# Kernel optimization log

Measured on AMD Instinct MI355X. Metric: run time of the kernel, lower is better.

The kernel has to match this reference:

```python
import jax, jax.numpy as jnp
import numpy as np

K = 7  # number of relaxed nearest neighbors (init arg k)
EXPM1_GUARD = 1e-7
LOG_HALF = float(np.log(0.5))

def log1mexp(x):
    # log(1 - exp(x)) for x <= 0, numerically stable (guard matches torch bw-path constant)
    t = x < LOG_HALF
    xa = jnp.where(t, x, -1.0)          # safe operand for log1p(-exp(.))
    xb = jnp.where(t, -1.0, x)          # safe operand for log(-expm1(.))
    ya = jnp.log1p(-jnp.exp(xa))
    yb = jnp.log(-jnp.expm1(xb) + EXPM1_GUARD)
    return jnp.where(t, ya, yb)

def setup_inputs() -> dict:
    key = jax.random.key(0)
    k1, k2, k3, k4 = jax.random.split(key, 4)
    b, n, m, o, e, f = 4, 8192, 2048, 64, 64, 128
    x = jax.random.normal(k1, (b, n, f), dtype=jnp.float32)
    xe = jax.random.normal(k2, (b, n, e), dtype=jnp.float32)
    ye = jax.random.normal(k3, (b, m, e), dtype=jnp.float32)
    log_temp_param = jnp.zeros((1,), dtype=jnp.float32)
    I = jax.random.randint(k4, (b, m, o), 0, n, dtype=jnp.int64)
    return {"x": x, "xe": xe, "ye": ye, "log_temp_param": log_temp_param, "I": I}

def reference(x, xe, ye, log_temp_param, I):
    b, n, f = x.shape
    m, o = I.shape[1], I.shape[2]
    bidx = jnp.arange(b)[:, None, None]          # [b,1,1] batch index for gathers

    # ---- compute_distances (indexed path): D[b,m,o] = -||xe[I] - ye||^2 ----
    xg_e = xe[bidx, I]                           # [b,m,o,e] gathered candidate embeddings
    diff = xg_e - ye[:, :, None, :]              # [b,m,o,e]
    D = -jnp.sum(diff * diff, axis=-1)           # [b,m,o]

    # ---- NeuralNearestNeighbors: temperature + k-step relaxed top-k ----
    temperature = jnp.exp(log_temp_param[0])     # log_temp_bias = log(1) = 0
    logits = (D / temperature).reshape(b * m, o)
    samples = []
    for _ in range(K):
        w = jax.nn.log_softmax(logits, axis=1)   # [b*m,o]
        samples.append(jnp.exp(w).reshape(b, m, o))
        logits = logits + log1mexp(w)
    W = jnp.stack(samples, axis=3)               # [b,m,o,K]

    # ---- aggregate_output: z[b,m,f,K] = sum_o W[b,m,o,K] * x[b, I[b,m,o], f] ----
    xg = x[bidx, I]                              # [b,m,o,f]
    z = jnp.einsum('bmok,bmof->bmfk', W, xg)     # [b,m,f,K]
    return z
```

## Files before the change

### kernel.cpp

```cpp
#include <hip/hip_runtime.h>
#include <math.h>

#define B_  4
#define N_  8192
#define M_  2048
#define O_  64
#define E_  64
#define F_  128
#define K_  7

__global__ __launch_bounds__(128, 6) void n3agg_kernel(
    const float* __restrict__ x, const float* __restrict__ xe,
    const float* __restrict__ ye, const float* __restrict__ log_temp,
    const int* __restrict__ I, float* __restrict__ out)
{
    __shared__ __align__(16) int   s_I[2][O_];
    __shared__ __align__(16) float s_ye[2][E_];
    __shared__ __align__(16) float s_W[2][O_][8];

    const int tid  = threadIdx.x;
    const int w    = tid >> 6;
    const int lane = tid & 63;
    const int bid  = blockIdx.x * 2 + w;
    const int b    = bid >> 11;

    const int my_idx = I[(size_t)bid * O_ + lane];
    s_I[w][lane]  = my_idx;
    s_ye[w][lane] = ye[(size_t)bid * E_ + lane];

    const float4* xr4 = (const float4*)(xe + ((size_t)b * N_ + my_idx) * E_);
    const float4* ye4 = (const float4*)(&s_ye[w][0]);
    float S[16];
    #pragma unroll
    for (int q = 0; q < 4; ++q) {
        float4 xa = xr4[q],      ya = ye4[q];
        float4 xb = xr4[q + 4],  yb = ye4[q + 4];
        float4 xc = xr4[q + 8],  yc = ye4[q + 8];
        float4 xd = xr4[q + 12], yd = ye4[q + 12];
        float da, db, dc, dd;

        da = __fsub_rn(xa.x, ya.x); db = __fsub_rn(xb.x, yb.x);
        dc = __fsub_rn(xc.x, yc.x); dd = __fsub_rn(xd.x, yd.x);
        S[4*q+0] = __fadd_rn(__fadd_rn(__fmul_rn(da,da), __fmul_rn(db,db)),
                             __fadd_rn(__fmul_rn(dc,dc), __fmul_rn(dd,dd)));

        da = __fsub_rn(xa.y, ya.y); db = __fsub_rn(xb.y, yb.y);
        dc = __fsub_rn(xc.y, yc.y); dd = __fsub_rn(xd.y, yd.y);
        S[4*q+1] = __fadd_rn(__fadd_rn(__fmul_rn(da,da), __fmul_rn(db,db)),
                             __fadd_rn(__fmul_rn(dc,dc), __fmul_rn(dd,dd)));

        da = __fsub_rn(xa.z, ya.z); db = __fsub_rn(xb.z, yb.z);
        dc = __fsub_rn(xc.z, yc.z); dd = __fsub_rn(xd.z, yd.z);
        S[4*q+2] = __fadd_rn(__fadd_rn(__fmul_rn(da,da), __fmul_rn(db,db)),
                             __fadd_rn(__fmul_rn(dc,dc), __fmul_rn(dd,dd)));

        da = __fsub_rn(xa.w, ya.w); db = __fsub_rn(xb.w, yb.w);
        dc = __fsub_rn(xc.w, yc.w); dd = __fsub_rn(xd.w, yd.w);
        S[4*q+3] = __fadd_rn(__fadd_rn(__fmul_rn(da,da), __fmul_rn(db,db)),
                             __fadd_rn(__fmul_rn(dc,dc), __fmul_rn(dd,dd)));
    }
    float t8[8], t4[4], t2[2], res;
    #pragma unroll
    for (int l = 0; l < 8; ++l) t8[l] = __fadd_rn(S[l], S[l + 8]);
    #pragma unroll
    for (int l = 0; l < 4; ++l) t4[l] = __fadd_rn(t8[l], t8[l + 4]);
    t2[0] = __fadd_rn(t4[0], t4[2]);
    t2[1] = __fadd_rn(t4[1], t4[3]);
    res   = __fadd_rn(t2[0], t2[1]);

    const float temp = expf(log_temp[0]);
    float logit = __fdiv_rn(-res, temp);

    float wreg[K_];
    #pragma unroll
    for (int k = 0; k < K_; ++k) {
        float mx = logit;
        #pragma unroll
        for (int d = 1; d < 64; d <<= 1) mx = fmaxf(mx, __shfl_xor(mx, d));
        float sh = __fsub_rn(logit, mx);
        float ex = expf(sh);
        float t = __fadd_rn(ex, __shfl_xor(ex, 16));
        t = __fadd_rn(t, __shfl_xor(t, 32));
        t = __fadd_rn(t, __shfl_xor(t, 8));
        t = __fadd_rn(t, __shfl_xor(t, 4));
        t = __fadd_rn(t, __shfl_xor(t, 2));
        t = __fadd_rn(t, __shfl_xor(t, 1));
        const float sm = t;

        float wv = __fsub_rn(sh, logf(sm));
        wreg[k] = expf(wv);

        float lm;
        if (wv < -0.69314718055994530942f) {
            lm = log1pf(-expf(wv));
        } else {
            lm = logf(__fadd_rn(-expm1f(wv), 1e-7f));
        }
        logit = __fadd_rn(logit, lm);
    }
    {
        float* wp = &s_W[w][lane][0];
        *(float4*)wp       = make_float4(wreg[0], wreg[1], wreg[2], wreg[3]);
        *(float2*)(wp + 4) = make_float2(wreg[4], wreg[5]);
        wp[6] = wreg[6];
    }

    const int h  = lane >> 5;
    const int fl = lane & 31;
    float acc[4][K_];
    #pragma unroll
    for (int q = 0; q < 4; ++q)
        #pragma unroll
        for (int k = 0; k < K_; ++k) acc[q][k] = 0.f;

    const float* xb = x + (size_t)b * N_ * F_ + 4 * fl;
    #pragma unroll 2
    for (int t = 0; t < 32; ++t) {
        const int o = 2 * t + h;
        const int idx = s_I[w][o];
        const float4 xv = *(const float4*)(xb + (size_t)idx * F_);
        const float* wrow = &s_W[w][o][0];
        const float4 wa = *(const float4*)(wrow);
        const float4 wb = *(const float4*)(wrow + 4);
        const float wk[K_] = {wa.x, wa.y, wa.z, wa.w, wb.x, wb.y, wb.z};
        #pragma unroll
        for (int k = 0; k < K_; ++k) {
            acc[0][k] = fmaf(wk[k], xv.x, acc[0][k]);
            acc[1][k] = fmaf(wk[k], xv.y, acc[1][k]);
            acc[2][k] = fmaf(wk[k], xv.z, acc[2][k]);
            acc[3][k] = fmaf(wk[k], xv.w, acc[3][k]);
        }
    }
    #pragma unroll
    for (int q = 0; q < 4; ++q)
        #pragma unroll
        for (int k = 0; k < K_; ++k)
            acc[q][k] += __shfl_xor(acc[q][k], 32);

    if (lane < 32) {
        const float* af = &acc[0][0];
        float4* op4 = (float4*)(out + (size_t)bid * F_ * K_ + fl * 28);
        #pragma unroll
        for (int j = 0; j < 7; ++j)
            op4[j] = make_float4(af[4*j], af[4*j+1], af[4*j+2], af[4*j+3]);
    }
}

extern "C" void kernel_launch(void* const* d_in, const int* in_sizes, int n_in,
                              void* d_out, int out_size, void* d_ws, size_t ws_size,
                              hipStream_t stream) {
    const float* x        = (const float*)d_in[0];
    const float* xe       = (const float*)d_in[1];
    const float* ye       = (const float*)d_in[2];
    const float* log_temp = (const float*)d_in[3];
    const int*   I        = (const int*)d_in[4];
    float* out = (float*)d_out;

    dim3 grid((B_ * M_) / 2);
    dim3 block(128);
    hipLaunchKernelGGL(n3agg_kernel, grid, block, 0, stream,
                       x, xe, ye, log_temp, I, out);
}
```

Measured before the change: 64.60 us.

## Split fused kernel into softmax and aggregation kernels via workspace

Splits the single fused kernel into a distance plus relaxed top-k kernel that writes W to workspace, followed by an aggregation kernel that reads W back. The aggregation kernel batches eight gathered x loads per step to raise memory-level parallelism. It stages output through LDS for coalesced stores, and both kernels remap block indices so blocks are spread across XCDs. The aim is to decouple the latency-bound softmax phase from the bandwidth-bound gather phase, at the cost of an extra global round trip for W and a second launch. The fused kernel is kept as a fallback when the workspace is too small.

```diff
diff --git a/kernel.cpp b/kernel.cpp
--- a/kernel.cpp
+++ b/kernel.cpp
@@ -9,23 +9,24 @@
 #define F_  128
 #define K_  7
 
-__global__ __launch_bounds__(128, 6) void n3agg_kernel(
-    const float* __restrict__ x, const float* __restrict__ xe,
-    const float* __restrict__ ye, const float* __restrict__ log_temp,
-    const int* __restrict__ I, float* __restrict__ out)
+__global__ __launch_bounds__(256, 8) void n3_softmax_kernel(
+    const float* __restrict__ xe, const float* __restrict__ ye,
+    const float* __restrict__ log_temp, const int* __restrict__ I,
+    float* __restrict__ W)
 {
-    __shared__ __align__(16) int   s_I[2][O_];
-    __shared__ __align__(16) float s_ye[2][E_];
-    __shared__ __align__(16) float s_W[2][O_][8];
+    __shared__ __align__(16) float s_ye[4][E_];
 
     const int tid  = threadIdx.x;
     const int w    = tid >> 6;
     const int lane = tid & 63;
-    const int bid  = blockIdx.x * 2 + w;
-    const int b    = bid >> 11;
+    const int nb    = gridDim.x;
+    const int chunk = nb >> 3;
+    const int blk   = blockIdx.x;
+    const int sb    = (blk & 7) * chunk + (blk >> 3);
+    const int bid   = sb * 4 + w;
+    const int b     = bid >> 11;
 
     const int my_idx = I[(size_t)bid * O_ + lane];
-    s_I[w][lane]  = my_idx;
     s_ye[w][lane] = ye[(size_t)bid * E_ + lane];
 
     const float4* xr4 = (const float4*)(xe + ((size_t)b * N_ + my_idx) * E_);
@@ -98,6 +99,175 @@
         }
         logit = __fadd_rn(logit, lm);
     }
+    float* wp = W + ((size_t)bid * O_ + lane) * 8;
+    *(float4*)wp       = make_float4(wreg[0], wreg[1], wreg[2], wreg[3]);
+    *(float2*)(wp + 4) = make_float2(wreg[4], wreg[5]);
+    wp[6] = wreg[6];
+}
+
+__global__ __launch_bounds__(128, 6) void n3_agg_kernel(
+    const float* __restrict__ x, const int* __restrict__ I,
+    const float* __restrict__ W, float* __restrict__ out)
+{
+    __shared__ __align__(16) int   s_I[2][O_];
+    __shared__ __align__(16) float s_W[2][O_][8];
+    __shared__ __align__(16) float s_o[2][896];
+
+    const int tid  = threadIdx.x;
+    const int w    = tid >> 6;
+    const int lane = tid & 63;
+    const int nb    = gridDim.x;
+    const int chunk = nb >> 3;
+    const int blk   = blockIdx.x;
+    const int sb    = (blk & 7) * chunk + (blk >> 3);
+    const int bid   = sb * 2 + w;
+    const int b     = bid >> 11;
+
+    s_I[w][lane] = I[(size_t)bid * O_ + lane];
+    const float4* wg = (const float4*)(W + (size_t)bid * (O_ * 8));
+    ((float4*)&s_W[w][0][0])[lane]      = wg[lane];
+    ((float4*)&s_W[w][0][0])[lane + 64] = wg[lane + 64];
+
+    const int h  = lane >> 5;
+    const int fl = lane & 31;
+    float acc[4][K_];
+    #pragma unroll
+    for (int q = 0; q < 4; ++q)
+        #pragma unroll
+        for (int k = 0; k < K_; ++k) acc[q][k] = 0.f;
+
+    const float* xb = x + (size_t)b * N_ * F_ + 4 * fl;
+    #pragma unroll
+    for (int tb = 0; tb < 4; ++tb) {
+        int idxv[8];
+        #pragma unroll
+        for (int j = 0; j < 8; ++j) idxv[j] = s_I[w][2 * (tb * 8 + j) + h];
+        float4 xv[8];
+        #pragma unroll
+        for (int j = 0; j < 8; ++j)
+            xv[j] = *(const float4*)(xb + (size_t)idxv[j] * F_);
+        #pragma unroll
+        for (int j = 0; j < 8; ++j) {
+            const int o = 2 * (tb * 8 + j) + h;
+            const float* wr = &s_W[w][o][0];
+            const float4 wa = *(const float4*)(wr);
+            const float4 wb2 = *(const float4*)(wr + 4);
+            const float wk[K_] = {wa.x, wa.y, wa.z, wa.w, wb2.x, wb2.y, wb2.z};
+            #pragma unroll
+            for (int k = 0; k < K_; ++k) {
+                acc[0][k] = fmaf(wk[k], xv[j].x, acc[0][k]);
+                acc[1][k] = fmaf(wk[k], xv[j].y, acc[1][k]);
+                acc[2][k] = fmaf(wk[k], xv[j].z, acc[2][k]);
+                acc[3][k] = fmaf(wk[k], xv[j].w, acc[3][k]);
+            }
+        }
+    }
+    #pragma unroll
+    for (int q = 0; q < 4; ++q)
+        #pragma unroll
+        for (int k = 0; k < K_; ++k)
+            acc[q][k] += __shfl_xor(acc[q][k], 32);
+
+    if (lane < 32) {
+        const float* af = &acc[0][0];
+        float* so = &s_o[w][fl * 28];
+        #pragma unroll
+        for (int j = 0; j < 7; ++j)
+            *(float4*)(so + 4 * j) = make_float4(af[4*j], af[4*j+1],
+                                                 af[4*j+2], af[4*j+3]);
+    }
+    float* ob = out + (size_t)bid * (F_ * K_);
+    #pragma unroll
+    for (int r = 0; r < 3; ++r) {
+        float4 v = ((const float4*)&s_o[w][0])[r * 64 + lane];
+        *(float4*)(ob + r * 256 + lane * 4) = v;
+    }
+    if (lane < 32) {
+        float4 v = ((const float4*)&s_o[w][0])[192 + lane];
+        *(float4*)(ob + 768 + lane * 4) = v;
+    }
+}
+
+__global__ __launch_bounds__(128, 6) void n3agg_fused_kernel(
+    const float* __restrict__ x, const float* __restrict__ xe,
+    const float* __restrict__ ye, const float* __restrict__ log_temp,
+    const int* __restrict__ I, float* __restrict__ out)
+{
+    __shared__ __align__(16) int   s_I[2][O_];
+    __shared__ __align__(16) float s_ye[2][E_];
+    __shared__ __align__(16) float s_W[2][O_][8];
+
+    const int tid  = threadIdx.x;
+    const int w    = tid >> 6;
+    const int lane = tid & 63;
+    const int bid  = blockIdx.x * 2 + w;
+    const int b    = bid >> 11;
+
+    const int my_idx = I[(size_t)bid * O_ + lane];
+    s_I[w][lane]  = my_idx;
+    s_ye[w][lane] = ye[(size_t)bid * E_ + lane];
+
+    const float4* xr4 = (const float4*)(xe + ((size_t)b * N_ + my_idx) * E_);
+    const float4* ye4 = (const float4*)(&s_ye[w][0]);
+    float S[16];
+    #pragma unroll
+    for (int q = 0; q < 4; ++q) {
+        float4 xa = xr4[q],      ya = ye4[q];
+        float4 xb = xr4[q + 4],  yb = ye4[q + 4];
+        float4 xc = xr4[q + 8],  yc = ye4[q + 8];
+        float4 xd = xr4[q + 12], yd = ye4[q + 12];
+        float da, db, dc, dd;
+        da = __fsub_rn(xa.x, ya.x); db = __fsub_rn(xb.x, yb.x);
+        dc = __fsub_rn(xc.x, yc.x); dd = __fsub_rn(xd.x, yd.x);
+        S[4*q+0] = __fadd_rn(__fadd_rn(__fmul_rn(da,da), __fmul_rn(db,db)),
+                             __fadd_rn(__fmul_rn(dc,dc), __fmul_rn(dd,dd)));
+        da = __fsub_rn(xa.y, ya.y); db = __fsub_rn(xb.y, yb.y);
+        dc = __fsub_rn(xc.y, yc.y); dd = __fsub_rn(xd.y, yd.y);
+        S[4*q+1] = __fadd_rn(__fadd_rn(__fmul_rn(da,da), __fmul_rn(db,db)),
+                             __fadd_rn(__fmul_rn(dc,dc), __fmul_rn(dd,dd)));
+        da = __fsub_rn(xa.z, ya.z); db = __fsub_rn(xb.z, yb.z);
+        dc = __fsub_rn(xc.z, yc.z); dd = __fsub_rn(xd.z, yd.z);
+        S[4*q+2] = __fadd_rn(__fadd_rn(__fmul_rn(da,da), __fmul_rn(db,db)),
+                             __fadd_rn(__fmul_rn(dc,dc), __fmul_rn(dd,dd)));
+        da = __fsub_rn(xa.w, ya.w); db = __fsub_rn(xb.w, yb.w);
+        dc = __fsub_rn(xc.w, yc.w); dd = __fsub_rn(xd.w, yd.w);
+        S[4*q+3] = __fadd_rn(__fadd_rn(__fmul_rn(da,da), __fmul_rn(db,db)),
+                             __fadd_rn(__fmul_rn(dc,dc), __fmul_rn(dd,dd)));
+    }
+    float t8[8], t4[4], t2[2], res;
+    #pragma unroll
+    for (int l = 0; l < 8; ++l) t8[l] = __fadd_rn(S[l], S[l + 8]);
+    #pragma unroll
+    for (int l = 0; l < 4; ++l) t4[l] = __fadd_rn(t8[l], t8[l + 4]);
+    t2[0] = __fadd_rn(t4[0], t4[2]);
+    t2[1] = __fadd_rn(t4[1], t4[3]);
+    res   = __fadd_rn(t2[0], t2[1]);
+
+    const float temp = expf(log_temp[0]);
+    float logit = __fdiv_rn(-res, temp);
+
+    float wreg[K_];
+    #pragma unroll
+    for (int k = 0; k < K_; ++k) {
+        float mx = logit;
+        #pragma unroll
+        for (int d = 1; d < 64; d <<= 1) mx = fmaxf(mx, __shfl_xor(mx, d));
+        float sh = __fsub_rn(logit, mx);
+        float ex = expf(sh);
+        float t = __fadd_rn(ex, __shfl_xor(ex, 16));
+        t = __fadd_rn(t, __shfl_xor(t, 32));
+        t = __fadd_rn(t, __shfl_xor(t, 8));
+        t = __fadd_rn(t, __shfl_xor(t, 4));
+        t = __fadd_rn(t, __shfl_xor(t, 2));
+        t = __fadd_rn(t, __shfl_xor(t, 1));
+        const float sm = t;
+        float wv = __fsub_rn(sh, logf(sm));
+        wreg[k] = expf(wv);
+        float lm;
+        if (wv < -0.69314718055994530942f) lm = log1pf(-expf(wv));
+        else lm = logf(__fadd_rn(-expm1f(wv), 1e-7f));
+        logit = __fadd_rn(logit, lm);
+    }
     {
         float* wp = &s_W[w][lane][0];
         *(float4*)wp       = make_float4(wreg[0], wreg[1], wreg[2], wreg[3]);
@@ -112,7 +282,6 @@
     for (int q = 0; q < 4; ++q)
         #pragma unroll
         for (int k = 0; k < K_; ++k) acc[q][k] = 0.f;
-
     const float* xb = x + (size_t)b * N_ * F_ + 4 * fl;
     #pragma unroll 2
     for (int t = 0; t < 32; ++t) {
@@ -136,7 +305,6 @@
         #pragma unroll
         for (int k = 0; k < K_; ++k)
             acc[q][k] += __shfl_xor(acc[q][k], 32);
-
     if (lane < 32) {
         const float* af = &acc[0][0];
         float4* op4 = (float4*)(out + (size_t)bid * F_ * K_ + fl * 28);
@@ -156,8 +324,15 @@
     const int*   I        = (const int*)d_in[4];
     float* out = (float*)d_out;
 
-    dim3 grid((B_ * M_) / 2);
-    dim3 block(128);
-    hipLaunchKernelGGL(n3agg_kernel, grid, block, 0, stream,
-                       x, xe, ye, log_temp, I, out);
+    const size_t w_need = (size_t)B_ * M_ * O_ * 8 * sizeof(float);
+    if (ws_size >= w_need) {
+        float* W = (float*)d_ws;
+        hipLaunchKernelGGL(n3_softmax_kernel, dim3((B_ * M_) / 4), dim3(256),
+                           0, stream, xe, ye, log_temp, I, W);
+        hipLaunchKernelGGL(n3_agg_kernel, dim3((B_ * M_) / 2), dim3(128),
+                           0, stream, x, I, W, out);
+    } else {
+        hipLaunchKernelGGL(n3agg_fused_kernel, dim3((B_ * M_) / 2), dim3(128),
+                           0, stream, x, xe, ye, log_temp, I, out);
+    }
 }
```

New measurement: 125.7 us. +94.6%, slower.

## Prefetch gathered x rows into registers before softmax and double-buffer aggregation

Applied to the files above, without the earlier changes.

Issues the gathered x row loads for the first half of the neighbors before the relaxed top-k softmax loop, so memory latency overlaps with transcendental math. The aggregation then alternates between two register buffers, refilling one while consuming the other. It also processes four query rows per 256-thread block and remaps block indices so consecutive rows are spread in chunks across XCDs. This adds significant register pressure and may lower occupancy.

```diff
diff --git a/kernel.cpp b/kernel.cpp
--- a/kernel.cpp
+++ b/kernel.cpp
@@ -9,20 +9,24 @@
 #define F_  128
 #define K_  7
 
-__global__ __launch_bounds__(128, 6) void n3agg_kernel(
+__global__ __launch_bounds__(256, 4) void n3agg_kernel(
     const float* __restrict__ x, const float* __restrict__ xe,
     const float* __restrict__ ye, const float* __restrict__ log_temp,
     const int* __restrict__ I, float* __restrict__ out)
 {
-    __shared__ __align__(16) int   s_I[2][O_];
-    __shared__ __align__(16) float s_ye[2][E_];
-    __shared__ __align__(16) float s_W[2][O_][8];
+    __shared__ __align__(16) int   s_I[4][O_];
+    __shared__ __align__(16) float s_ye[4][E_];
+    __shared__ __align__(16) float s_W[4][O_][8];
 
     const int tid  = threadIdx.x;
     const int w    = tid >> 6;
     const int lane = tid & 63;
-    const int bid  = blockIdx.x * 2 + w;
-    const int b    = bid >> 11;
+    const int nb    = gridDim.x;
+    const int chunk = nb >> 3;
+    const int blk   = blockIdx.x;
+    const int sb    = (blk & 7) * chunk + (blk >> 3);
+    const int bid   = sb * 4 + w;
+    const int b     = bid >> 11;
 
     const int my_idx = I[(size_t)bid * O_ + lane];
     s_I[w][lane]  = my_idx;
@@ -34,27 +38,27 @@
     #pragma unroll
     for (int q = 0; q < 4; ++q) {
         float4 xa = xr4[q],      ya = ye4[q];
-        float4 xb = xr4[q + 4],  yb = ye4[q + 4];
+        float4 xb2 = xr4[q + 4],  yb = ye4[q + 4];
         float4 xc = xr4[q + 8],  yc = ye4[q + 8];
         float4 xd = xr4[q + 12], yd = ye4[q + 12];
         float da, db, dc, dd;
 
-        da = __fsub_rn(xa.x, ya.x); db = __fsub_rn(xb.x, yb.x);
+        da = __fsub_rn(xa.x, ya.x); db = __fsub_rn(xb2.x, yb.x);
         dc = __fsub_rn(xc.x, yc.x); dd = __fsub_rn(xd.x, yd.x);
         S[4*q+0] = __fadd_rn(__fadd_rn(__fmul_rn(da,da), __fmul_rn(db,db)),
                              __fadd_rn(__fmul_rn(dc,dc), __fmul_rn(dd,dd)));
 
-        da = __fsub_rn(xa.y, ya.y); db = __fsub_rn(xb.y, yb.y);
+        da = __fsub_rn(xa.y, ya.y); db = __fsub_rn(xb2.y, yb.y);
         dc = __fsub_rn(xc.y, yc.y); dd = __fsub_rn(xd.y, yd.y);
         S[4*q+1] = __fadd_rn(__fadd_rn(__fmul_rn(da,da), __fmul_rn(db,db)),
                              __fadd_rn(__fmul_rn(dc,dc), __fmul_rn(dd,dd)));
 
-        da = __fsub_rn(xa.z, ya.z); db = __fsub_rn(xb.z, yb.z);
+        da = __fsub_rn(xa.z, ya.z); db = __fsub_rn(xb2.z, yb.z);
         dc = __fsub_rn(xc.z, yc.z); dd = __fsub_rn(xd.z, yd.z);
         S[4*q+2] = __fadd_rn(__fadd_rn(__fmul_rn(da,da), __fmul_rn(db,db)),
                              __fadd_rn(__fmul_rn(dc,dc), __fmul_rn(dd,dd)));
 
-        da = __fsub_rn(xa.w, ya.w); db = __fsub_rn(xb.w, yb.w);
+        da = __fsub_rn(xa.w, ya.w); db = __fsub_rn(xb2.w, yb.w);
         dc = __fsub_rn(xc.w, yc.w); dd = __fsub_rn(xd.w, yd.w);
         S[4*q+3] = __fadd_rn(__fadd_rn(__fmul_rn(da,da), __fmul_rn(db,db)),
                              __fadd_rn(__fmul_rn(dc,dc), __fmul_rn(dd,dd)));
@@ -70,6 +74,18 @@
 
     const float temp = expf(log_temp[0]);
     float logit = __fdiv_rn(-res, temp);
+
+    const int h  = lane >> 5;
+    const int fl = lane & 31;
+    const float* xb = x + (size_t)b * N_ * F_ + 4 * fl;
+    float4 xvA[8], xvB[8];
+    #pragma unroll
+    for (int j = 0; j < 8; ++j)
+        xvA[j] = *(const float4*)(xb + (size_t)s_I[w][2 * j + h] * F_);
+    #pragma unroll
+    for (int j = 0; j < 8; ++j)
+        xvB[j] = *(const float4*)(xb + (size_t)s_I[w][2 * (8 + j) + h] * F_);
+    __builtin_amdgcn_sched_barrier(0);
 
     float wreg[K_];
     #pragma unroll
@@ -105,32 +121,44 @@
         wp[6] = wreg[6];
     }
 
-    const int h  = lane >> 5;
-    const int fl = lane & 31;
     float acc[4][K_];
     #pragma unroll
     for (int q = 0; q < 4; ++q)
         #pragma unroll
         for (int k = 0; k < K_; ++k) acc[q][k] = 0.f;
 
-    const float* xb = x + (size_t)b * N_ * F_ + 4 * fl;
-    #pragma unroll 2
-    for (int t = 0; t < 32; ++t) {
-        const int o = 2 * t + h;
-        const int idx = s_I[w][o];
-        const float4 xv = *(const float4*)(xb + (size_t)idx * F_);
-        const float* wrow = &s_W[w][o][0];
-        const float4 wa = *(const float4*)(wrow);
-        const float4 wb = *(const float4*)(wrow + 4);
-        const float wk[K_] = {wa.x, wa.y, wa.z, wa.w, wb.x, wb.y, wb.z};
-        #pragma unroll
-        for (int k = 0; k < K_; ++k) {
-            acc[0][k] = fmaf(wk[k], xv.x, acc[0][k]);
-            acc[1][k] = fmaf(wk[k], xv.y, acc[1][k]);
-            acc[2][k] = fmaf(wk[k], xv.z, acc[2][k]);
-            acc[3][k] = fmaf(wk[k], xv.w, acc[3][k]);
-        }
-    }
+#define CONSUME(XV, TB) do {                                                  \
+    _Pragma("unroll")                                                         \
+    for (int j = 0; j < 8; ++j) {                                             \
+        const int o = 2 * ((TB) * 8 + j) + h;                                 \
+        const float* wr = &s_W[w][o][0];                                      \
+        const float4 wa = *(const float4*)(wr);                               \
+        const float4 wb2 = *(const float4*)(wr + 4);                          \
+        const float wk[K_] = {wa.x, wa.y, wa.z, wa.w, wb2.x, wb2.y, wb2.z};   \
+        _Pragma("unroll")                                                     \
+        for (int k = 0; k < K_; ++k) {                                        \
+            acc[0][k] = fmaf(wk[k], XV[j].x, acc[0][k]);                      \
+            acc[1][k] = fmaf(wk[k], XV[j].y, acc[1][k]);                      \
+            acc[2][k] = fmaf(wk[k], XV[j].z, acc[2][k]);                      \
+            acc[3][k] = fmaf(wk[k], XV[j].w, acc[3][k]);                      \
+        }                                                                     \
+    }                                                                         \
+} while (0)
+
+#define REFILL(XV, TB) do {                                                   \
+    _Pragma("unroll")                                                         \
+    for (int j = 0; j < 8; ++j)                                               \
+        XV[j] = *(const float4*)(xb + (size_t)s_I[w][2 * ((TB) * 8 + j) + h] * F_); \
+} while (0)
+
+    CONSUME(xvA, 0); REFILL(xvA, 2);
+    CONSUME(xvB, 1); REFILL(xvB, 3);
+    CONSUME(xvA, 2);
+    CONSUME(xvB, 3);
+
+#undef CONSUME
+#undef REFILL
+
     #pragma unroll
     for (int q = 0; q < 4; ++q)
         #pragma unroll
@@ -156,8 +184,8 @@
     const int*   I        = (const int*)d_in[4];
     float* out = (float*)d_out;
 
-    dim3 grid((B_ * M_) / 2);
-    dim3 block(128);
+    dim3 grid((B_ * M_) / 4);
+    dim3 block(256);
     hipLaunchKernelGGL(n3agg_kernel, grid, block, 0, stream,
                        x, xe, ye, log_temp, I, out);
 }
```

After: 176.7 us. +173.6%, slower.
